# Kernel tuning notes

Measured on AMD Instinct MI355X. Metric: run time of the kernel, lower is better.

## Reference

```python
import jax, jax.numpy as jnp
import numpy as np

B, T, C_IN = 2, 4096, 1024
INTER, OUT = 1024, 1024
ROPE_DIM = 64
GAMMA = 0.99609375  # 1 - 2**-8
GROUPS = 32
EPS = 1e-6


def setup_inputs() -> dict:
    key = jax.random.key(0)
    k = jax.random.split(key, 4)
    return {
        "X_Q": jax.random.normal(k[0], (B, T, C_IN), dtype=jnp.float32),
        "W_Q": jax.random.normal(k[1], (C_IN, INTER), dtype=jnp.float32) / C_IN,
        "W_K": jax.random.normal(k[2], (C_IN, INTER), dtype=jnp.float32) / C_IN,
        "W_V": jax.random.normal(k[3], (C_IN, OUT), dtype=jnp.float32) / C_IN,
        "gn_weight": jnp.ones((OUT,), dtype=jnp.float32),
        "gn_bias": jnp.zeros((OUT,), dtype=jnp.float32),
    }


def _rope(x):
    # lucidrains RotaryEmbedding: rotate first ROPE_DIM features, pairwise-adjacent
    t = x.shape[-2]
    inv_freq = 1.0 / (10000.0 ** (jnp.arange(0, ROPE_DIM, 2, dtype=jnp.float32) / ROPE_DIM))
    freqs = jnp.arange(t, dtype=jnp.float32)[:, None] * inv_freq[None, :]  # [T, ROPE_DIM/2]
    freqs = jnp.repeat(freqs, 2, axis=-1)                                   # [T, ROPE_DIM]
    cos, sin = jnp.cos(freqs), jnp.sin(freqs)
    xr, xp = x[..., :ROPE_DIM], x[..., ROPE_DIM:]
    x1, x2 = xr[..., 0::2], xr[..., 1::2]
    rot = jnp.stack([-x2, x1], axis=-1).reshape(xr.shape)  # rotate_half (adjacent pairs)
    return jnp.concatenate([xr * cos + rot * sin, xp], axis=-1)


def _group_norm(x, w, b):
    # torch GroupNorm applied on x.reshape(-1, C)
    sh = x.shape
    c = sh[-1]
    xr = x.reshape(-1, GROUPS, c // GROUPS)
    mu = xr.mean(-1, keepdims=True)
    var = xr.var(-1, keepdims=True)
    xn = ((xr - mu) * jax.lax.rsqrt(var + EPS)).reshape(-1, c)
    return (xn * w + b).reshape(sh)


def reference(X_Q, W_Q, W_K, W_V, gn_weight, gn_bias):
    Q = jax.nn.silu(_rope(X_Q @ W_Q))  # [B,T,INTER]
    K = jax.nn.silu(_rope(X_Q @ W_K))
    V = jax.nn.silu(X_Q @ W_V)         # [B,T,OUT]
    A = jnp.einsum('btd,bsd->bts', Q, K)  # [B,T,T]
    # decay mask: original multiplies by _get_D(gamma,T).T -> gamma^(m-n) for m>=n
    n = jnp.arange(T)[:, None]
    m = jnp.arange(T)[None, :]
    upper = m >= n
    Dt = jnp.where(upper, GAMMA ** jnp.where(upper, m - n, 0).astype(jnp.float32), 0.0)
    A = A * Dt
    out = jnp.einsum('bts,bsd->btd', A, V)  # [B,T,OUT]
    # dropout p=0 (eval) -> identity
    return _group_norm(out, gn_weight, gn_bias)
```

## Files before the change

kernel.cpp:

```cpp
#include <hip/hip_runtime.h>


typedef __attribute__((ext_vector_type(8))) short bf16x8;
typedef __attribute__((ext_vector_type(4))) short bf16x4;
typedef __attribute__((ext_vector_type(4))) float f32x4;

#define MFMA16(a, b, c) __builtin_amdgcn_mfma_f32_16x16x32_bf16(a, b, c, 0, 0, 0)

static __device__ __forceinline__ short f2bf(float f) {
  unsigned u = __builtin_bit_cast(unsigned, f);
  u = (u + 0x7fffu + ((u >> 16) & 1u)) >> 16;
  return (short)u;
}

static __device__ __forceinline__ void gl_lds16(const void* g, void* l) {
  __builtin_amdgcn_global_load_lds(
      (const __attribute__((address_space(1))) void*)g,
      (__attribute__((address_space(3))) void*)l, 16, 0, 0);
}

#define T_LEN 4096
#define CIN 1024

#define LOG2G (-0.0056465633f)
#define L2IF (0.41524101f)

__global__ __launch_bounds__(256)
void convert_x(const float* __restrict__ X, short* __restrict__ Xb) {
  const size_t id = (size_t)blockIdx.x * 256 + threadIdx.x;
  float4 f = *(const float4*)&X[id * 4];
  bf16x4 v = {f2bf(f.x), f2bf(f.y), f2bf(f.z), f2bf(f.w)};
  *(bf16x4*)&Xb[id * 4] = v;
}

__global__ __launch_bounds__(256)
void transpose_w(const float* __restrict__ Wq, const float* __restrict__ Wk,
                 const float* __restrict__ Wv, short* __restrict__ WT) {
  const int k0 = blockIdx.x * 64, n0 = blockIdx.y * 64, mat = blockIdx.z;
  const float* __restrict__ W = (mat == 0) ? Wq : (mat == 1) ? Wk : Wv;
  __shared__ short tile[64][72];
  const int tid = threadIdx.x;
  const int r = tid >> 4, c = tid & 15;
#pragma unroll
  for (int i = 0; i < 4; ++i) {
    int row = r + 16 * i;
    float4 f = *(const float4*)&W[(size_t)(k0 + row) * CIN + n0 + c * 4];
    tile[c * 4 + 0][row] = f2bf(f.x);
    tile[c * 4 + 1][row] = f2bf(f.y);
    tile[c * 4 + 2][row] = f2bf(f.z);
    tile[c * 4 + 3][row] = f2bf(f.w);
  }
  __syncthreads();
  const int n = tid >> 2, seg = tid & 3;
  bf16x8 lo = *(const bf16x8*)&tile[n][seg * 16];
  bf16x8 hi = *(const bf16x8*)&tile[n][seg * 16 + 8];
  short* dst = &WT[(size_t)(mat * 1024 + n0 + n) * CIN + k0 + seg * 16];
  *(bf16x8*)dst = lo;
  *(bf16x8*)(dst + 8) = hi;
}

#define GEMM_DECLS()                                   \
  const int tid = threadIdx.x;                         \
  const int lane = tid & 63, wave = tid >> 6;          \
  const int wm = wave >> 1, wn = wave & 1;             \
  const int l15 = lane & 15, quad = lane >> 4;         \
  const int srow = wave * 8 + (lane >> 3);             \
  const int scol = (lane & 7) * 8;                     \
  const int ssw = (((lane & 7) ^ (lane >> 3)) * 8);    \
  const int asw = (l15 & 7);

#define ACC_INIT4(acc)                                 \
  _Pragma("unroll") for (int i = 0; i < 4; ++i)        \
  _Pragma("unroll") for (int j = 0; j < 4; ++j) {      \
    f32x4 z = {0.f, 0.f, 0.f, 0.f};                    \
    acc[i][j] = z;                                     \
  }

#define STAGE_TILE(dst, src, ld, r0, k0, nrows)        \
  _Pragma("unroll") for (int i = 0; i < (nrows) / 32; ++i) \
    gl_lds16(&src[(size_t)((r0) + i * 32 + srow) * (ld) + (k0) + ssw], \
             &dst[i * 32 + srow][scol]);

#define FRAG_MFMA44(As, Bs, acc)                                            \
  {                                                                         \
    bf16x8 af[4][2], bfr[4][2];                                             \
    _Pragma("unroll") for (int im = 0; im < 4; ++im)                        \
    _Pragma("unroll") for (int ks = 0; ks < 2; ++ks)                        \
      af[im][ks] = *(const bf16x8*)&As[wm * 64 + im * 16 + l15]             \
                       [((ks * 4 + quad) ^ asw) * 8];                       \
    _Pragma("unroll") for (int in = 0; in < 4; ++in)                        \
    _Pragma("unroll") for (int ks = 0; ks < 2; ++ks)                        \
      bfr[in][ks] = *(const bf16x8*)&Bs[wn * 64 + in * 16 + l15]            \
                        [((ks * 4 + quad) ^ asw) * 8];                      \
    _Pragma("unroll") for (int ks = 0; ks < 2; ++ks)                        \
    _Pragma("unroll") for (int im = 0; im < 4; ++im)                        \
    _Pragma("unroll") for (int in = 0; in < 4; ++in)                        \
      acc[im][in] = MFMA16(af[im][ks], bfr[in][ks], acc[im][in]);           \
  }

__global__ __launch_bounds__(256, 2)
void qkv_gemm(const short* __restrict__ Xb, const short* __restrict__ WT,
              short* __restrict__ Qb, short* __restrict__ Kb,
              short* __restrict__ Vt) {
  __shared__ __align__(16) short As[128][64];
  __shared__ __align__(16) short Bs[128][64];
  GEMM_DECLS();
  const int m0 = blockIdx.x * 128;
  const int c0 = blockIdx.y * 128;

  f32x4 acc[4][4];
  ACC_INIT4(acc);

  for (int k0 = 0; k0 < CIN; k0 += 64) {
    __syncthreads();
    STAGE_TILE(As, Xb, CIN, m0, k0, 128);
    STAGE_TILE(Bs, WT, CIN, c0, k0, 128);
    __syncthreads();
    FRAG_MFMA44(As, Bs, acc);
  }

  const int mat = (c0 >> 10);
#pragma unroll
  for (int im = 0; im < 4; ++im) {
#pragma unroll
    for (int in = 0; in < 4; ++in) {
      const int c = c0 + wn * 64 + in * 16 + l15;
      const int colm = c & 1023;
      const bool rope = (mat < 2) && (colm < 64);
      const float invf = exp2f(-L2IF * (float)(colm >> 1));
      const int mbase = m0 + wm * 64 + im * 16 + quad * 4;
      short vv[4];
#pragma unroll
      for (int r = 0; r < 4; ++r) {
        float v = acc[im][in][r];
        int m = mbase + r;
        int t = m & (T_LEN - 1);
        float partner = __shfl_xor(v, 1, 64);
        if (rope) {
          float ang = (float)t * invf;
          float s_, c_;
          sincosf(ang, &s_, &c_);
          v = (colm & 1) ? (v * c_ + partner * s_) : (v * c_ - partner * s_);
        }
        v = v / (1.f + __expf(-v));
        vv[r] = f2bf(v);
      }
      if (mat == 0) {
#pragma unroll
        for (int r = 0; r < 4; ++r) Qb[(size_t)(mbase + r) * 1024 + colm] = vv[r];
      } else if (mat == 1) {
#pragma unroll
        for (int r = 0; r < 4; ++r) Kb[(size_t)(mbase + r) * 1024 + colm] = vv[r];
      } else {
        bf16x4 v4 = {vv[0], vv[1], vv[2], vv[3]};
        *(bf16x4*)&Vt[(size_t)colm * 8192 + mbase] = v4;
      }
    }
  }
}

__global__ __launch_bounds__(256, 2)
void score_kernel(const short* __restrict__ Qb, const short* __restrict__ Kb,
                  short* __restrict__ Ab) {
  int idx = blockIdx.x;
  int ti = 0;
  while (idx >= 32 - ti) { idx -= 32 - ti; ++ti; }
  const int si = ti + idx;
  const int b = blockIdx.y;
  const int s0 = si * 128, t0 = ti * 128;

  __shared__ __align__(16) short Qs[128][64];
  __shared__ __align__(16) short Ks[128][64];
  GEMM_DECLS();

  f32x4 acc[4][4];
  ACC_INIT4(acc);

  for (int k0 = 0; k0 < 1024; k0 += 64) {
    __syncthreads();
    STAGE_TILE(Qs, Qb, 1024, b * T_LEN + t0, k0, 128);
    STAGE_TILE(Ks, Kb, 1024, b * T_LEN + s0, k0, 128);
    __syncthreads();
    FRAG_MFMA44(Qs, Ks, acc);
  }

#pragma unroll
  for (int im = 0; im < 4; ++im) {
#pragma unroll
    for (int in = 0; in < 4; ++in) {
      int s = s0 + wn * 64 + in * 16 + l15;
#pragma unroll
      for (int r = 0; r < 4; ++r) {
        int t = t0 + wm * 64 + im * 16 + quad * 4 + r;
        int d = s - t;
        float v = acc[im][in][r];
        v = (d < 0) ? 0.f : v * exp2f((float)d * LOG2G);
        Ab[((size_t)(b * T_LEN + t)) * T_LEN + s] = f2bf(v);
      }
    }
  }
}

__global__ __launch_bounds__(256, 2)
void av_kernel(const short* __restrict__ Ab, const short* __restrict__ Vt,
               float* __restrict__ Out) {
  const int p = blockIdx.x, b = blockIdx.y, di = blockIdx.z;
  const int n0 = di * 128;

  __shared__ __align__(16) short As2[64][64];
  __shared__ __align__(16) short Vs[128][64];
  GEMM_DECLS();

#pragma unroll 1
  for (int half = 0; half < 2; ++half) {
    const int ti2 = half ? (63 - p) : p;
    const int t0 = ti2 * 64;

    f32x4 acc[2][4];
#pragma unroll
    for (int i = 0; i < 2; ++i)
#pragma unroll
      for (int j = 0; j < 4; ++j) {
        f32x4 z = {0.f, 0.f, 0.f, 0.f};
        acc[i][j] = z;
      }

    for (int s = t0; s < T_LEN; s += 64) {
      __syncthreads();
      STAGE_TILE(As2, Ab, T_LEN, b * T_LEN + t0, s, 64);
      STAGE_TILE(Vs, Vt, 8192, n0, b * T_LEN + s, 128);
      __syncthreads();
      bf16x8 af[2][2], bfr[4][2];
#pragma unroll
      for (int im = 0; im < 2; ++im)
#pragma unroll
        for (int ks = 0; ks < 2; ++ks)
          af[im][ks] = *(const bf16x8*)&As2[wm * 32 + im * 16 + l15]
                           [((ks * 4 + quad) ^ asw) * 8];
#pragma unroll
      for (int in = 0; in < 4; ++in)
#pragma unroll
        for (int ks = 0; ks < 2; ++ks)
          bfr[in][ks] = *(const bf16x8*)&Vs[wn * 64 + in * 16 + l15]
                            [((ks * 4 + quad) ^ asw) * 8];
#pragma unroll
      for (int ks = 0; ks < 2; ++ks)
#pragma unroll
        for (int im = 0; im < 2; ++im)
#pragma unroll
          for (int in = 0; in < 4; ++in)
            acc[im][in] = MFMA16(af[im][ks], bfr[in][ks], acc[im][in]);
    }

#pragma unroll
    for (int im = 0; im < 2; ++im) {
#pragma unroll
      for (int in = 0; in < 4; ++in) {
        int n = n0 + wn * 64 + in * 16 + l15;
#pragma unroll
        for (int r = 0; r < 4; ++r) {
          int t = t0 + wm * 32 + im * 16 + quad * 4 + r;
          Out[((size_t)(b * T_LEN + t)) * 1024 + n] = acc[im][in][r];
        }
      }
    }
  }
}

__global__ __launch_bounds__(256)
void gn_kernel(float* __restrict__ Out, const float* __restrict__ gw,
               const float* __restrict__ gb) {
  const int row = blockIdx.x;
  const int tid = threadIdx.x;
  const int ch0 = tid * 4;
  float4 v = *(const float4*)&Out[(size_t)row * 1024 + ch0];
  float s = v.x + v.y + v.z + v.w;
  float q = v.x * v.x + v.y * v.y + v.z * v.z + v.w * v.w;
  s += __shfl_xor(s, 1, 64);
  q += __shfl_xor(q, 1, 64);
  s += __shfl_xor(s, 2, 64);
  q += __shfl_xor(q, 2, 64);
  s += __shfl_xor(s, 4, 64);
  q += __shfl_xor(q, 4, 64);
  float mean = s * (1.f / 32.f);
  float var = q * (1.f / 32.f) - mean * mean;
  float rstd = rsqrtf(var + 1e-6f);
  float4 o;
  o.x = (v.x - mean) * rstd * gw[ch0 + 0] + gb[ch0 + 0];
  o.y = (v.y - mean) * rstd * gw[ch0 + 1] + gb[ch0 + 1];
  o.z = (v.z - mean) * rstd * gw[ch0 + 2] + gb[ch0 + 2];
  o.w = (v.w - mean) * rstd * gw[ch0 + 3] + gb[ch0 + 3];
  *(float4*)&Out[(size_t)row * 1024 + ch0] = o;
}

extern "C" void kernel_launch(void* const* d_in, const int* in_sizes, int n_in,
                              void* d_out, int out_size, void* d_ws,
                              size_t ws_size, hipStream_t stream) {
  const float* X = (const float*)d_in[0];
  const float* Wq = (const float*)d_in[1];
  const float* Wk = (const float*)d_in[2];
  const float* Wv = (const float*)d_in[3];
  const float* gw = (const float*)d_in[4];
  const float* gb = (const float*)d_in[5];
  float* Out = (float*)d_out;

  short* Qb = (short*)d_ws;
  short* Kb = Qb + (size_t)8192 * 1024;
  short* Vt = Kb + (size_t)8192 * 1024;
  short* Ab = Vt + (size_t)8192 * 1024;
  short* Xb = Ab;
  short* WT = Xb + (size_t)8192 * 1024;

  convert_x<<<8192, 256, 0, stream>>>(X, Xb);
  transpose_w<<<dim3(16, 16, 3), 256, 0, stream>>>(Wq, Wk, Wv, WT);
  qkv_gemm<<<dim3(64, 24), 256, 0, stream>>>(Xb, WT, Qb, Kb, Vt);
  score_kernel<<<dim3(528, 2), 256, 0, stream>>>(Qb, Kb, Ab);
  av_kernel<<<dim3(32, 2, 8), 256, 0, stream>>>(Ab, Vt, Out);
  gn_kernel<<<8192, 256, 0, stream>>>(Out, gw, gb);
}
```

Before: 309.0 us.

## Replace direct global-to-LDS loads with register-prefetched double stage in GEMM kernels

In all three GEMM-style kernels, the direct global_load_lds staging is replaced by loads into registers. Each thread prefetches the next K tile into registers while the MFMA work on the current LDS tile runs, then writes the registers to swizzled LDS at the start of the next iteration. The aim is to hide global memory latency behind compute, which the old load-then-sync-then-compute loop could not do. The cost is extra VGPRs for the prefetch buffers, which may hurt occupancy under launch_bounds(256,2), plus an explicit LDS write pass.

New measurement: 921.9 us. 2.98x slower.

```diff
diff --git a/kernel.cpp b/kernel.cpp
--- a/kernel.cpp
+++ b/kernel.cpp
@@ -11,12 +11,6 @@
   unsigned u = __builtin_bit_cast(unsigned, f);
   u = (u + 0x7fffu + ((u >> 16) & 1u)) >> 16;
   return (short)u;
-}
-
-static __device__ __forceinline__ void gl_lds16(const void* g, void* l) {
-  __builtin_amdgcn_global_load_lds(
-      (const __attribute__((address_space(1))) void*)g,
-      (__attribute__((address_space(3))) void*)l, 16, 0, 0);
 }
 
 #define T_LEN 4096
@@ -64,9 +58,9 @@
   const int lane = tid & 63, wave = tid >> 6;          \
   const int wm = wave >> 1, wn = wave & 1;             \
   const int l15 = lane & 15, quad = lane >> 4;         \
-  const int srow = wave * 8 + (lane >> 3);             \
-  const int scol = (lane & 7) * 8;                     \
-  const int ssw = (((lane & 7) ^ (lane >> 3)) * 8);    \
+  const int srow = tid >> 3;                           \
+  const int schunk = tid & 7;                          \
+  const int swz = schunk ^ (srow & 7);                 \
   const int asw = (l15 & 7);
 
 #define ACC_INIT4(acc)                                 \
@@ -76,10 +70,14 @@
     acc[i][j] = z;                                     \
   }
 
-#define STAGE_TILE(dst, src, ld, r0, k0, nrows)        \
-  _Pragma("unroll") for (int i = 0; i < (nrows) / 32; ++i) \
-    gl_lds16(&src[(size_t)((r0) + i * 32 + srow) * (ld) + (k0) + ssw], \
-             &dst[i * 32 + srow][scol]);
+#define LOAD_TILE(reg, src, ld, r0, k0, nrows)                          \
+  _Pragma("unroll") for (int i = 0; i < (nrows) / 32; ++i)              \
+    reg[i] = *(const uint4*)&src[(size_t)((r0) + i * 32 + srow) * (ld) + \
+                                 (k0) + schunk * 8];
+
+#define WRITE_TILE(dst, reg, nrows)                                     \
+  _Pragma("unroll") for (int i = 0; i < (nrows) / 32; ++i)              \
+    *(uint4*)&dst[i * 32 + srow][swz * 8] = reg[i];
 
 #define FRAG_MFMA44(As, Bs, acc)                                            \
   {                                                                         \
@@ -111,12 +109,20 @@
   f32x4 acc[4][4];
   ACC_INIT4(acc);
 
+  uint4 ra[4], rb[4];
+  LOAD_TILE(ra, Xb, CIN, m0, 0, 128);
+  LOAD_TILE(rb, WT, CIN, c0, 0, 128);
+
   for (int k0 = 0; k0 < CIN; k0 += 64) {
+    WRITE_TILE(As, ra, 128);
+    WRITE_TILE(Bs, rb, 128);
     __syncthreads();
-    STAGE_TILE(As, Xb, CIN, m0, k0, 128);
-    STAGE_TILE(Bs, WT, CIN, c0, k0, 128);
+    if (k0 + 64 < CIN) {
+      LOAD_TILE(ra, Xb, CIN, m0, k0 + 64, 128);
+      LOAD_TILE(rb, WT, CIN, c0, k0 + 64, 128);
+    }
+    FRAG_MFMA44(As, Bs, acc);
     __syncthreads();
-    FRAG_MFMA44(As, Bs, acc);
   }
 
   const int mat = (c0 >> 10);
@@ -176,12 +182,20 @@
   f32x4 acc[4][4];
   ACC_INIT4(acc);
 
+  uint4 ra[4], rb[4];
+  LOAD_TILE(ra, Qb, 1024, b * T_LEN + t0, 0, 128);
+  LOAD_TILE(rb, Kb, 1024, b * T_LEN + s0, 0, 128);
+
   for (int k0 = 0; k0 < 1024; k0 += 64) {
+    WRITE_TILE(Qs, ra, 128);
+    WRITE_TILE(Ks, rb, 128);
     __syncthreads();
-    STAGE_TILE(Qs, Qb, 1024, b * T_LEN + t0, k0, 128);
-    STAGE_TILE(Ks, Kb, 1024, b * T_LEN + s0, k0, 128);
+    if (k0 + 64 < 1024) {
+      LOAD_TILE(ra, Qb, 1024, b * T_LEN + t0, k0 + 64, 128);
+      LOAD_TILE(rb, Kb, 1024, b * T_LEN + s0, k0 + 64, 128);
+    }
+    FRAG_MFMA44(Qs, Ks, acc);
     __syncthreads();
-    FRAG_MFMA44(Qs, Ks, acc);
   }
 
 #pragma unroll
@@ -225,11 +239,18 @@
         acc[i][j] = z;
       }
 
+    uint4 ra[2], rb[4];
+    LOAD_TILE(ra, Ab, T_LEN, b * T_LEN + t0, t0, 64);
+    LOAD_TILE(rb, Vt, 8192, n0, b * T_LEN + t0, 128);
+
     for (int s = t0; s < T_LEN; s += 64) {
+      WRITE_TILE(As2, ra, 64);
+      WRITE_TILE(Vs, rb, 128);
       __syncthreads();
-      STAGE_TILE(As2, Ab, T_LEN, b * T_LEN + t0, s, 64);
-      STAGE_TILE(Vs, Vt, 8192, n0, b * T_LEN + s, 128);
-      __syncthreads();
+      if (s + 64 < T_LEN) {
+        LOAD_TILE(ra, Ab, T_LEN, b * T_LEN + t0, s + 64, 64);
+        LOAD_TILE(rb, Vt, 8192, n0, b * T_LEN + s + 64, 128);
+      }
       bf16x8 af[2][2], bfr[4][2];
 #pragma unroll
       for (int im = 0; im < 2; ++im)
@@ -250,6 +271,7 @@
 #pragma unroll
           for (int in = 0; in < 4; ++in)
             acc[im][in] = MFMA16(af[im][ks], bfr[in][ks], acc[im][in]);
+      __syncthreads();
     }
 
 #pragma unroll
```

## Pre-swizzle intermediate buffers in global memory so LDS staging loads are contiguous

Applied to the files above, without the earlier changes.

Every producer (convert_x, transpose_w, QKV epilogue, score epilogue) now writes its bf16 output with the XOR swizzle already applied within each 64-element chunk. The staging loads into LDS can then read contiguous 16-byte segments per row instead of computing swizzled global addresses. The aim is better global-load coalescing for the direct-to-LDS loads. It also widens convert_x to 8 elements per thread with half the blocks. The risk is that scattered swizzled scalar stores in the Q/K/A epilogues may reduce write coalescing, and every consumer must agree on the layout.

After: 318.5 us. 1.03x slower.

```diff
diff --git a/kernel.cpp b/kernel.cpp
--- a/kernel.cpp
+++ b/kernel.cpp
@@ -19,6 +19,10 @@
       (__attribute__((address_space(3))) void*)l, 16, 0, 0);
 }
 
+static __device__ __forceinline__ int swzc(int col, int row) {
+  return (((col >> 3) ^ (row & 7)) << 3) | (col & 7);
+}
+
 #define T_LEN 4096
 #define CIN 1024
 
@@ -27,10 +31,16 @@
 
 __global__ __launch_bounds__(256)
 void convert_x(const float* __restrict__ X, short* __restrict__ Xb) {
-  const size_t id = (size_t)blockIdx.x * 256 + threadIdx.x;
-  float4 f = *(const float4*)&X[id * 4];
-  bf16x4 v = {f2bf(f.x), f2bf(f.y), f2bf(f.z), f2bf(f.w)};
-  *(bf16x4*)&Xb[id * 4] = v;
+  const int gid = blockIdx.x * 256 + threadIdx.x;
+  const int row = gid >> 7;
+  const int c = gid & 127;
+  const float* s = &X[(size_t)gid * 8];
+  float4 f0 = *(const float4*)s;
+  float4 f1 = *(const float4*)(s + 4);
+  bf16x8 v = {f2bf(f0.x), f2bf(f0.y), f2bf(f0.z), f2bf(f0.w),
+              f2bf(f1.x), f2bf(f1.y), f2bf(f1.z), f2bf(f1.w)};
+  const int pc = (c & 0x78) | ((c ^ row) & 7);
+  *(bf16x8*)&Xb[(size_t)row * 1024 + pc * 8] = v;
 }
 
 __global__ __launch_bounds__(256)
@@ -54,9 +64,11 @@
   const int n = tid >> 2, seg = tid & 3;
   bf16x8 lo = *(const bf16x8*)&tile[n][seg * 16];
   bf16x8 hi = *(const bf16x8*)&tile[n][seg * 16 + 8];
-  short* dst = &WT[(size_t)(mat * 1024 + n0 + n) * CIN + k0 + seg * 16];
-  *(bf16x8*)dst = lo;
-  *(bf16x8*)(dst + 8) = hi;
+  const int R = mat * 1024 + n0 + n;
+  const int a0 = (k0 >> 3) + seg * 2;
+  short* base = &WT[(size_t)R * CIN];
+  *(bf16x8*)&base[(a0 ^ (n & 7)) * 8] = lo;
+  *(bf16x8*)&base[((a0 + 1) ^ (n & 7)) * 8] = hi;
 }
 
 #define GEMM_DECLS()                                   \
@@ -64,9 +76,8 @@
   const int lane = tid & 63, wave = tid >> 6;          \
   const int wm = wave >> 1, wn = wave & 1;             \
   const int l15 = lane & 15, quad = lane >> 4;         \
-  const int srow = wave * 8 + (lane >> 3);             \
-  const int scol = (lane & 7) * 8;                     \
-  const int ssw = (((lane & 7) ^ (lane >> 3)) * 8);    \
+  const int srow = tid >> 3;                           \
+  const int scol = (tid & 7) * 8;                      \
   const int asw = (l15 & 7);
 
 #define ACC_INIT4(acc)                                 \
@@ -78,7 +89,7 @@
 
 #define STAGE_TILE(dst, src, ld, r0, k0, nrows)        \
   _Pragma("unroll") for (int i = 0; i < (nrows) / 32; ++i) \
-    gl_lds16(&src[(size_t)((r0) + i * 32 + srow) * (ld) + (k0) + ssw], \
+    gl_lds16(&src[(size_t)((r0) + i * 32 + srow) * (ld) + (k0) + scol], \
              &dst[i * 32 + srow][scol]);
 
 #define FRAG_MFMA44(As, Bs, acc)                                            \
@@ -147,13 +158,16 @@
       }
       if (mat == 0) {
 #pragma unroll
-        for (int r = 0; r < 4; ++r) Qb[(size_t)(mbase + r) * 1024 + colm] = vv[r];
+        for (int r = 0; r < 4; ++r)
+          Qb[(size_t)(mbase + r) * 1024 + swzc(colm, mbase + r)] = vv[r];
       } else if (mat == 1) {
 #pragma unroll
-        for (int r = 0; r < 4; ++r) Kb[(size_t)(mbase + r) * 1024 + colm] = vv[r];
+        for (int r = 0; r < 4; ++r)
+          Kb[(size_t)(mbase + r) * 1024 + swzc(colm, mbase + r)] = vv[r];
       } else {
         bf16x4 v4 = {vv[0], vv[1], vv[2], vv[3]};
-        *(bf16x4*)&Vt[(size_t)colm * 8192 + mbase] = v4;
+        *(bf16x4*)&Vt[(size_t)colm * 8192 +
+                      (((mbase >> 3) ^ (colm & 7)) << 3) + (mbase & 7)] = v4;
       }
     }
   }
@@ -195,7 +209,7 @@
         int d = s - t;
         float v = acc[im][in][r];
         v = (d < 0) ? 0.f : v * exp2f((float)d * LOG2G);
-        Ab[((size_t)(b * T_LEN + t)) * T_LEN + s] = f2bf(v);
+        Ab[((size_t)(b * T_LEN + t)) * T_LEN + swzc(s, t)] = f2bf(v);
       }
     }
   }
@@ -311,7 +325,7 @@
   short* Xb = Ab;
   short* WT = Xb + (size_t)8192 * 1024;
 
-  convert_x<<<8192, 256, 0, stream>>>(X, Xb);
+  convert_x<<<4096, 256, 0, stream>>>(X, Xb);
   transpose_w<<<dim3(16, 16, 3), 256, 0, stream>>>(Wq, Wk, Wv, WT);
   qkv_gemm<<<dim3(64, 24), 256, 0, stream>>>(Xb, WT, Qb, Kb, Vt);
   score_kernel<<<dim3(528, 2), 256, 0, stream>>>(Qb, Kb, Ab);
```
